# Performance work log

Hardware: AMD Instinct MI355X
Metric: run time of the kernel (lower is better)

The kernel has to match this reference:

```python
import jax, jax.numpy as jnp
import numpy as np

N_NODES = 100000
N_EDGES = 3200000
N_FEAT = 128
HIDDEN = 16
N_CLASSES = 10
N_GRAPHS = 64


def gcn_conv(x, W, b, src, dst, num_nodes):
    # PyG GCNConv: h = x W; add self-loops; norm = deg^{-1/2}[src]*deg^{-1/2}[dst]
    h = x @ W  # [N, out]
    deg = jax.ops.segment_sum(jnp.ones(src.shape[0], h.dtype), dst,
                              num_segments=num_nodes) + 1.0  # self-loop
    dinv = jax.lax.rsqrt(deg)
    coef = dinv[src] * dinv[dst]  # [E]
    agg = jax.ops.segment_sum(h[src] * coef[:, None], dst,
                              num_segments=num_nodes)
    # self-loop contribution: norm = dinv[i]^2
    agg = agg + h * (dinv * dinv)[:, None]
    return agg + b


def setup_inputs() -> dict:
    key = jax.random.key(0)
    k1, k2, k3, k4, k5, k6, k7 = jax.random.split(key, 7)
    x = jax.random.normal(k1, (N_NODES, N_FEAT), dtype=jnp.float32)
    edge_index = jax.random.randint(k2, (2, N_EDGES), 0, N_NODES, dtype=jnp.int64)
    batch = jnp.sort(jax.random.randint(k3, (N_NODES,), 0, N_GRAPHS, dtype=jnp.int64))
    W1 = jax.random.normal(k4, (N_FEAT, HIDDEN), dtype=jnp.float32) / np.sqrt(N_FEAT)
    b1 = jnp.zeros((HIDDEN,), jnp.float32)
    W2 = jax.random.normal(k5, (HIDDEN, N_CLASSES), dtype=jnp.float32) / np.sqrt(HIDDEN)
    b2 = jnp.zeros((N_CLASSES,), jnp.float32)
    return {"x": x, "edge_index": edge_index, "batch": batch,
            "W1": W1, "b1": b1, "W2": W2, "b2": b2}


def reference(x, edge_index, batch, W1, b1, W2, b2):
    src, dst = edge_index[0], edge_index[1]
    h = gcn_conv(x, W1, b1, src, dst, N_NODES)
    h = jax.nn.relu(h)
    h = gcn_conv(h, W2, b2, src, dst, N_NODES)  # [N, C]
    # global mean pool per graph
    sums = jax.ops.segment_sum(h, batch, num_segments=N_GRAPHS)
    cnts = jax.ops.segment_sum(jnp.ones(N_NODES, h.dtype), batch,
                               num_segments=N_GRAPHS)
    pooled = sums / jnp.maximum(cnts, 1.0)[:, None]  # [G, C]
    return jax.nn.log_softmax(pooled, axis=1)
```

## Files before the change

### kernel.cpp

```cpp
#include <hip/hip_runtime.h>
#include <hip/hip_fp16.h>

#define N_NODES   100000
#define N_EDGES   3200000
#define N_FEAT    128
#define HIDDEN    16
#define N_CLASSES 10
#define N_GRAPHS  64

#define NBUCK     391
#define CAP       9216
#define BINA_EPB  16384
#define BINA_BLOCKS ((N_EDGES + BINA_EPB - 1) / BINA_EPB)


__global__ __launch_bounds__(512) void k_ginit(int* __restrict__ gcur,
                                               float* __restrict__ pooled) {
    int t = threadIdx.x;
    if (t < NBUCK) gcur[t] = t * CAP;
    pooled[t] = 0.f;
    pooled[t + 512] = 0.f;
}

__global__ __launch_bounds__(1024) void k_binA(const int* __restrict__ src,
                                               const int* __restrict__ dst,
                                               int* __restrict__ gcur,
                                               int* __restrict__ stage) {
    __shared__ int hist[NBUCK];
    __shared__ int curb[NBUCK];
    int tid = threadIdx.x;
    long long base = (long long)blockIdx.x * BINA_EPB;
    for (int t = tid; t < NBUCK; t += 1024) hist[t] = 0;
    __syncthreads();
    int se[16], de[16];
#pragma unroll
    for (int i = 0; i < 16; ++i) {
        long long e = base + i * 1024 + tid;
        if (e < N_EDGES) {
            se[i] = src[e];
            de[i] = dst[e];
            atomicAdd(&hist[de[i] >> 8], 1);
        } else {
            de[i] = -1;
        }
    }
    __syncthreads();
    for (int t = tid; t < NBUCK; t += 1024) {
        int h = hist[t];
        curb[t] = h ? atomicAdd(&gcur[t], h) : 0;
    }
    __syncthreads();
#pragma unroll
    for (int i = 0; i < 16; ++i) {
        if (de[i] >= 0) {
            int b = de[i] >> 8;
            int p = atomicAdd(&curb[b], 1);
            stage[p] = (se[i] << 8) | (de[i] & 255);
        }
    }
}

__global__ __launch_bounds__(512) void k_bscan(const int* __restrict__ gcur,
                                               int* __restrict__ bbase,
                                               int* __restrict__ off) {
    __shared__ int s[512];
    int t = threadIdx.x;
    int c = (t < NBUCK) ? (gcur[t] - t * CAP) : 0;
    s[t] = c;
    __syncthreads();
    for (int o = 1; o < 512; o <<= 1) {
        int a = (t >= o) ? s[t - o] : 0;
        __syncthreads();
        s[t] += a;
        __syncthreads();
    }
    if (t < NBUCK) bbase[t] = s[t] - c;
    if (t == 0) off[N_NODES] = N_EDGES;
}

__global__ __launch_bounds__(256) void k_binB(const int* __restrict__ gcur,
                                              const int* __restrict__ bbase,
                                              const int* __restrict__ stage,
                                              int* __restrict__ off,
                                              float* __restrict__ dinv,
                                              int* __restrict__ srcs) {
    __shared__ int hist[256];
    __shared__ int excl[256];
    int b = blockIdx.x, t = threadIdx.x;
    int cnt   = gcur[b] - b * CAP;
    int sbase = b * CAP;
    int cbase = bbase[b];
    hist[t] = 0;
    __syncthreads();
    for (int i = t; i < cnt; i += 256) {
        int v = stage[sbase + i];
        atomicAdd(&hist[v & 255], 1);
    }
    __syncthreads();
    int c = hist[t];
    excl[t] = c;
    __syncthreads();
    for (int o = 1; o < 256; o <<= 1) {
        int a = (t >= o) ? excl[t - o] : 0;
        __syncthreads();
        excl[t] += a;
        __syncthreads();
    }
    int ex = excl[t] - c;
    int node = b * 256 + t;
    if (node < N_NODES) {
        off[node]  = cbase + ex;
        dinv[node] = rsqrtf((float)c + 1.0f);
    }
    __syncthreads();
    hist[t] = ex;
    __syncthreads();
    for (int i = t; i < cnt; i += 256) {
        int v = stage[sbase + i];
        int p = cbase + atomicAdd(&hist[v & 255], 1);
        srcs[p] = v >> 8;
    }
}

__global__ __launch_bounds__(256) void k_gemm1(const float* __restrict__ x,
                                               const float* __restrict__ W1,
                                               const float* __restrict__ dinv,
                                               __half* __restrict__ h1h) {
    __shared__ float w[N_FEAT * HIDDEN];
    __shared__ float xs[16 * N_FEAT];
    __shared__ float ds[16];
    int tid  = threadIdx.x;
    int base = blockIdx.x * 16;
    if (tid < 16) ds[tid] = dinv[base + tid];
    const float4* w4 = (const float4*)W1;
    float4*       wd = (float4*)w;
    wd[tid]       = w4[tid];
    wd[256 + tid] = w4[256 + tid];
    const float4* x4 = (const float4*)(x + (long long)base * N_FEAT);
    float4*       xd = (float4*)xs;
    xd[tid]       = x4[tid];
    xd[256 + tid] = x4[256 + tid];
    __syncthreads();
    int n = tid >> 4, c = tid & 15;
    const float* xr = &xs[n * N_FEAT];
    float acc = 0.f;
#pragma unroll
    for (int k = 0; k < N_FEAT; ++k) acc += xr[k] * w[k * HIDDEN + c];
    h1h[(base + n) * HIDDEN + c] = __float2half(acc * ds[n]);
}

#define NT(p) __builtin_nontemporal_load(p)

#define GATHER_DEF(TBL)                                                       \
    float acc[8];                                                             \
    _Pragma("unroll") for (int q = 0; q < 8; ++q) acc[q] = 0.f;               \
    {                                                                         \
        int ne = end - beg;                                                   \
        int nr = ne >> 3;                                                     \
        int j  = beg + k;                                                     \
        int npair = nr >> 1;                                                  \
        if (npair > 0) {                                                      \
            int sA = NT(&srcs[j]), sB = NT(&srcs[j + 8]);                     \
            for (int p = 1; p < npair; ++p) {                                 \
                int sC = NT(&srcs[j + 16]), sD = NT(&srcs[j + 24]);           \
                GACC(TBL, sA); GACC(TBL, sB);                                 \
                sA = sC; sB = sD; j += 16;                                    \
            }                                                                 \
            GACC(TBL, sA); GACC(TBL, sB); j += 16;                            \
        }                                                                     \
        if (nr & 1) { int sA = NT(&srcs[j]); GACC(TBL, sA); j += 8; }         \
        if (k < (ne & 7)) { int sA = NT(&srcs[j]); GACC(TBL, sA); }           \
    }                                                                         \
    _Pragma("unroll") for (int m = 2; m <= 8; m <<= 1) {                      \
        _Pragma("unroll") for (int q = 0; q < 8; ++q)                         \
            acc[q] += __shfl_xor(acc[q], m, 64);                              \
    }

#define GACC(TBL, S) {                                                        \
    float4 g_ = *(const float4*)(&TBL[(S) * 16 + h * 8]);                     \
    const __half2* hp_ = (const __half2*)&g_;                                 \
    float2 v0_ = __half22float2(hp_[0]);                                      \
    float2 v1_ = __half22float2(hp_[1]);                                      \
    float2 v2_ = __half22float2(hp_[2]);                                      \
    float2 v3_ = __half22float2(hp_[3]);                                      \
    acc[0] += v0_.x; acc[1] += v0_.y; acc[2] += v1_.x; acc[3] += v1_.y;       \
    acc[4] += v2_.x; acc[5] += v2_.y; acc[6] += v3_.x; acc[7] += v3_.y; }

__global__ __launch_bounds__(256) void k_agg1(const int* __restrict__ off,
                                              const int* __restrict__ srcs,
                                              const float* __restrict__ dinv,
                                              const __half* __restrict__ h1h,
                                              const float* __restrict__ b1,
                                              const float* __restrict__ W2,
                                              __half* __restrict__ h2h) {
    __shared__ float r_s[16][17];
    __shared__ float w2s[HIDDEN * N_CLASSES];
    int tid = threadIdx.x;
    if (tid < HIDDEN * N_CLASSES) w2s[tid] = W2[tid];
    int nl = tid >> 4, l = tid & 15, k = l >> 1, h = l & 1;
    int n  = blockIdx.x * 16 + nl;
    int beg = off[n], end = off[n + 1];
    GATHER_DEF(h1h)
    if (l < 2) {
#pragma unroll
        for (int q = 0; q < 8; ++q) r_s[nl][h * 8 + q] = acc[q];
    }
    __syncthreads();
    float dn   = dinv[n];
    float self = __half2float(h1h[n * 16 + l]);
    float val  = fmaxf(dn * (r_s[nl][l] + self) + b1[l], 0.f);
    __syncthreads();
    r_s[nl][l] = val;
    __syncthreads();
    float o = 0.f;
    if (l < N_CLASSES) {
#pragma unroll
        for (int q = 0; q < HIDDEN; ++q) o += r_s[nl][q] * w2s[q * N_CLASSES + l];
        o *= dn;
    }
    h2h[n * 16 + l] = __float2half(o);
}

__global__ __launch_bounds__(256) void k_agg2p(const int* __restrict__ off,
                                               const int* __restrict__ srcs,
                                               const float* __restrict__ dinv,
                                               const __half* __restrict__ h2h,
                                               const int* __restrict__ batch,
                                               float* __restrict__ pooled) {
    __shared__ float red[16][17];
    int tid = threadIdx.x;
    int nl = tid >> 4, l = tid & 15, k = l >> 1, h = l & 1;
    int nbase = blockIdx.x * 16;
    int n  = nbase + nl;
    int beg = off[n], end = off[n + 1];
    GATHER_DEF(h2h)
    if (l < 2) {
#pragma unroll
        for (int q = 0; q < 8; ++q) red[nl][h * 8 + q] = acc[q];
    }
    __syncthreads();
    float self = __half2float(h2h[n * 16 + l]);
    float o = dinv[n] * (red[nl][l] + self);
    __syncthreads();

    int g0  = batch[nbase];
    int g15 = batch[nbase + 15];
    if (g0 == g15) {
        red[nl][l] = o;
        __syncthreads();
#pragma unroll
        for (int s = 8; s > 0; s >>= 1) {
            if (nl < s) red[nl][l] += red[nl + s][l];
            __syncthreads();
        }
        if (tid < N_CLASSES) atomicAdd(&pooled[g0 * 16 + tid], red[0][tid]);
    } else {
        if (l < N_CLASSES) atomicAdd(&pooled[batch[n] * 16 + l], o);
    }
}

__global__ __launch_bounds__(64) void k_final(const float* __restrict__ pooled,
                                              const float* __restrict__ b2,
                                              const int* __restrict__ batch,
                                              float* __restrict__ out) {
    int g = threadIdx.x;
    if (g >= N_GRAPHS) return;
    int lo = 0, hi = N_NODES;
    while (lo < hi) { int m = (lo + hi) >> 1; if (batch[m] < g) lo = m + 1; else hi = m; }
    int start = lo;
    lo = 0; hi = N_NODES;
    while (lo < hi) { int m = (lo + hi) >> 1; if (batch[m] < g + 1) lo = m + 1; else hi = m; }
    int cnt = lo - start;

    float v[N_CLASSES];
    if (cnt > 0) {
        float inv = 1.f / (float)cnt;
#pragma unroll
        for (int j = 0; j < N_CLASSES; ++j) v[j] = pooled[g * 16 + j] * inv + b2[j];
    } else {
#pragma unroll
        for (int j = 0; j < N_CLASSES; ++j) v[j] = 0.f;
    }
    float m = v[0];
#pragma unroll
    for (int j = 1; j < N_CLASSES; ++j) m = fmaxf(m, v[j]);
    float l = 0.f;
#pragma unroll
    for (int j = 0; j < N_CLASSES; ++j) l += expf(v[j] - m);
    l = logf(l);
#pragma unroll
    for (int j = 0; j < N_CLASSES; ++j) out[g * N_CLASSES + j] = v[j] - m - l;
}

extern "C" void kernel_launch(void* const* d_in, const int* in_sizes, int n_in,
                              void* d_out, int out_size, void* d_ws, size_t ws_size,
                              hipStream_t stream) {
    const float* x     = (const float*)d_in[0];
    const int*   edge  = (const int*)d_in[1];
    const int*   batch = (const int*)d_in[2];
    const float* W1    = (const float*)d_in[3];
    const float* b1    = (const float*)d_in[4];
    const float* W2    = (const float*)d_in[5];
    const float* b2    = (const float*)d_in[6];
    float* out = (float*)d_out;
    float* ws  = (float*)d_ws;

    int*    gcur   = (int*)ws;
    int*    bbase  = (int*)(ws + 512);
    float*  pooled = ws + 1024;
    float*  dinv   = ws + 2048;
    int*    off    = (int*)(ws + 102048);
    int*    srcs   = (int*)(ws + 202080);
    int*    stage  = (int*)(ws + 3402080);
    __half* h1h    = (__half*)(ws + 3402080);
    __half* h2h    = (__half*)(ws + 4202080);

    const int* srcp = edge;
    const int* dstp = edge + N_EDGES;

    k_ginit<<<1, 512, 0, stream>>>(gcur, pooled);
    k_binA<<<BINA_BLOCKS, 1024, 0, stream>>>(srcp, dstp, gcur, stage);
    k_bscan<<<1, 512, 0, stream>>>(gcur, bbase, off);
    k_binB<<<NBUCK, 256, 0, stream>>>(gcur, bbase, stage, off, dinv, srcs);
    k_gemm1<<<N_NODES / 16, 256, 0, stream>>>(x, W1, dinv, h1h);
    k_agg1<<<N_NODES / 16, 256, 0, stream>>>(off, srcs, dinv, h1h, b1, W2, h2h);
    k_agg2p<<<N_NODES / 16, 256, 0, stream>>>(off, srcs, dinv, h2h, batch, pooled);
    k_final<<<1, 64, 0, stream>>>(pooled, b2, batch, out);
}
```

Baseline: 249.1 us.

## Drop bucket scan kernel, use padded per-bucket CSR with begin/end pairs

Removes the single-block bucket prefix-scan launch by keeping each bucket's edges at its fixed CAP-strided slot and storing an explicit (begin,end) pair per node instead of a compact offset array. The binning kernel now uses 512 threads and int4 vectorized reads of the staging buffer. This saves one kernel launch and its serialization point, at the cost of a sparser srcs layout, a larger workspace and an extra 8-byte load per node in the aggregation kernels.

```diff
diff --git a/kernel.cpp b/kernel.cpp
--- a/kernel.cpp
+++ b/kernel.cpp
@@ -60,65 +60,70 @@
     }
 }
 
-__global__ __launch_bounds__(512) void k_bscan(const int* __restrict__ gcur,
-                                               int* __restrict__ bbase,
-                                               int* __restrict__ off) {
-    __shared__ int s[512];
-    int t = threadIdx.x;
-    int c = (t < NBUCK) ? (gcur[t] - t * CAP) : 0;
-    s[t] = c;
-    __syncthreads();
-    for (int o = 1; o < 512; o <<= 1) {
-        int a = (t >= o) ? s[t - o] : 0;
-        __syncthreads();
-        s[t] += a;
-        __syncthreads();
-    }
-    if (t < NBUCK) bbase[t] = s[t] - c;
-    if (t == 0) off[N_NODES] = N_EDGES;
-}
-
-__global__ __launch_bounds__(256) void k_binB(const int* __restrict__ gcur,
-                                              const int* __restrict__ bbase,
+__global__ __launch_bounds__(512) void k_binB(const int* __restrict__ gcur,
                                               const int* __restrict__ stage,
-                                              int* __restrict__ off,
+                                              int2* __restrict__ be,
                                               float* __restrict__ dinv,
                                               int* __restrict__ srcs) {
     __shared__ int hist[256];
     __shared__ int excl[256];
-    int b = blockIdx.x, t = threadIdx.x;
+    int b = blockIdx.x, tid = threadIdx.x;
     int cnt   = gcur[b] - b * CAP;
     int sbase = b * CAP;
-    int cbase = bbase[b];
-    hist[t] = 0;
-    __syncthreads();
-    for (int i = t; i < cnt; i += 256) {
-        int v = stage[sbase + i];
+    if (tid < 256) hist[tid] = 0;
+    __syncthreads();
+    int nvec = cnt >> 2;
+    for (int i = tid; i < nvec; i += 512) {
+        int4 v = *(const int4*)&stage[sbase + i * 4];
+        atomicAdd(&hist[v.x & 255], 1);
+        atomicAdd(&hist[v.y & 255], 1);
+        atomicAdd(&hist[v.z & 255], 1);
+        atomicAdd(&hist[v.w & 255], 1);
+    }
+    if (tid < (cnt & 3)) {
+        int v = stage[sbase + (nvec << 2) + tid];
         atomicAdd(&hist[v & 255], 1);
     }
     __syncthreads();
-    int c = hist[t];
-    excl[t] = c;
+    int c = 0, ex = 0;
+    if (tid < 256) {
+        c = hist[tid];
+        excl[tid] = c;
+    }
     __syncthreads();
     for (int o = 1; o < 256; o <<= 1) {
-        int a = (t >= o) ? excl[t - o] : 0;
+        int a = 0;
+        if (tid < 256 && tid >= o) a = excl[tid - o];
         __syncthreads();
-        excl[t] += a;
+        if (tid < 256) excl[tid] += a;
         __syncthreads();
     }
-    int ex = excl[t] - c;
-    int node = b * 256 + t;
-    if (node < N_NODES) {
-        off[node]  = cbase + ex;
-        dinv[node] = rsqrtf((float)c + 1.0f);
-    }
-    __syncthreads();
-    hist[t] = ex;
-    __syncthreads();
-    for (int i = t; i < cnt; i += 256) {
-        int v = stage[sbase + i];
-        int p = cbase + atomicAdd(&hist[v & 255], 1);
-        srcs[p] = v >> 8;
+    if (tid < 256) {
+        ex = excl[tid] - c;
+        int node = b * 256 + tid;
+        if (node < N_NODES) {
+            be[node]   = make_int2(sbase + ex, sbase + ex + c);
+            dinv[node] = rsqrtf((float)c + 1.0f);
+        }
+    }
+    __syncthreads();
+    if (tid < 256) hist[tid] = ex;
+    __syncthreads();
+    for (int i = tid; i < nvec; i += 512) {
+        int4 v = *(const int4*)&stage[sbase + i * 4];
+        int p0 = atomicAdd(&hist[v.x & 255], 1);
+        int p1 = atomicAdd(&hist[v.y & 255], 1);
+        int p2 = atomicAdd(&hist[v.z & 255], 1);
+        int p3 = atomicAdd(&hist[v.w & 255], 1);
+        srcs[sbase + p0] = v.x >> 8;
+        srcs[sbase + p1] = v.y >> 8;
+        srcs[sbase + p2] = v.z >> 8;
+        srcs[sbase + p3] = v.w >> 8;
+    }
+    if (tid < (cnt & 3)) {
+        int v = stage[sbase + (nvec << 2) + tid];
+        int p = atomicAdd(&hist[v & 255], 1);
+        srcs[sbase + p] = v >> 8;
     }
 }
 
@@ -186,7 +191,7 @@
     acc[0] += v0_.x; acc[1] += v0_.y; acc[2] += v1_.x; acc[3] += v1_.y;       \
     acc[4] += v2_.x; acc[5] += v2_.y; acc[6] += v3_.x; acc[7] += v3_.y; }
 
-__global__ __launch_bounds__(256) void k_agg1(const int* __restrict__ off,
+__global__ __launch_bounds__(256) void k_agg1(const int2* __restrict__ be,
                                               const int* __restrict__ srcs,
                                               const float* __restrict__ dinv,
                                               const __half* __restrict__ h1h,
@@ -199,7 +204,8 @@
     if (tid < HIDDEN * N_CLASSES) w2s[tid] = W2[tid];
     int nl = tid >> 4, l = tid & 15, k = l >> 1, h = l & 1;
     int n  = blockIdx.x * 16 + nl;
-    int beg = off[n], end = off[n + 1];
+    int2 bn = be[n];
+    int beg = bn.x, end = bn.y;
     GATHER_DEF(h1h)
     if (l < 2) {
 #pragma unroll
@@ -221,7 +227,7 @@
     h2h[n * 16 + l] = __float2half(o);
 }
 
-__global__ __launch_bounds__(256) void k_agg2p(const int* __restrict__ off,
+__global__ __launch_bounds__(256) void k_agg2p(const int2* __restrict__ be,
                                                const int* __restrict__ srcs,
                                                const float* __restrict__ dinv,
                                                const __half* __restrict__ h2h,
@@ -232,7 +238,8 @@
     int nl = tid >> 4, l = tid & 15, k = l >> 1, h = l & 1;
     int nbase = blockIdx.x * 16;
     int n  = nbase + nl;
-    int beg = off[n], end = off[n + 1];
+    int2 bn = be[n];
+    int beg = bn.x, end = bn.y;
     GATHER_DEF(h2h)
     if (l < 2) {
 #pragma unroll
@@ -306,24 +313,22 @@
     float* ws  = (float*)d_ws;
 
     int*    gcur   = (int*)ws;
-    int*    bbase  = (int*)(ws + 512);
-    float*  pooled = ws + 1024;
-    float*  dinv   = ws + 2048;
-    int*    off    = (int*)(ws + 102048);
-    int*    srcs   = (int*)(ws + 202080);
-    int*    stage  = (int*)(ws + 3402080);
-    __half* h1h    = (__half*)(ws + 3402080);
-    __half* h2h    = (__half*)(ws + 4202080);
+    float*  pooled = ws + 512;
+    float*  dinv   = ws + 1536;
+    int2*   be     = (int2*)(ws + 101536);
+    int*    srcs   = (int*)(ws + 301536);
+    int*    stage  = (int*)(ws + 3904992);
+    __half* h1h    = (__half*)(ws + 3904992);
+    __half* h2h    = (__half*)(ws + 4704992);
 
     const int* srcp = edge;
     const int* dstp = edge + N_EDGES;
 
     k_ginit<<<1, 512, 0, stream>>>(gcur, pooled);
     k_binA<<<BINA_BLOCKS, 1024, 0, stream>>>(srcp, dstp, gcur, stage);
-    k_bscan<<<1, 512, 0, stream>>>(gcur, bbase, off);
-    k_binB<<<NBUCK, 256, 0, stream>>>(gcur, bbase, stage, off, dinv, srcs);
+    k_binB<<<NBUCK, 512, 0, stream>>>(gcur, stage, be, dinv, srcs);
     k_gemm1<<<N_NODES / 16, 256, 0, stream>>>(x, W1, dinv, h1h);
-    k_agg1<<<N_NODES / 16, 256, 0, stream>>>(off, srcs, dinv, h1h, b1, W2, h2h);
-    k_agg2p<<<N_NODES / 16, 256, 0, stream>>>(off, srcs, dinv, h2h, batch, pooled);
+    k_agg1<<<N_NODES / 16, 256, 0, stream>>>(be, srcs, dinv, h1h, b1, W2, h2h);
+    k_agg2p<<<N_NODES / 16, 256, 0, stream>>>(be, srcs, dinv, h2h, batch, pooled);
     k_final<<<1, 64, 0, stream>>>(pooled, b2, batch, out);
 }
```

Measured after the change: 238.6 us. -4.2%, faster.
